# Kernel tuning notes

Measured on AMD Instinct MI355X. Metric: run time of the kernel, lower is better.

The kernel has to match this reference:

```python
import jax, jax.numpy as jnp
import numpy as np

N_EMB = 2048
EMB_DIM = 512
EPS_IN = 1e-5  # instance-norm epsilon (torch default used in instance_norm)


def setup_inputs() -> dict:
    key = jax.random.key(0)
    kx, ke = jax.random.split(key)
    x = jax.random.normal(kx, (32, 1024, EMB_DIM), dtype=jnp.float32)
    # codebook init: uniform(-1/M, 1/M), then row-normalized (as in __init__)
    init_bound = 1.0 / N_EMB
    emb = jax.random.uniform(ke, (N_EMB, EMB_DIM), dtype=jnp.float32,
                             minval=-init_bound, maxval=init_bound)
    emb = emb / (jnp.linalg.norm(emb, axis=1, keepdims=True) + 1e-4)
    return {"x": x, "embedding": emb}


def _instance_norm(x, axis, eps=EPS_IN):
    mu = jnp.mean(x, axis=axis, keepdims=True)
    # torch.std default is unbiased (ddof=1)
    std = jnp.std(x, axis=axis, keepdims=True, ddof=1)
    return (x - mu) / (std + eps)


def reference(x, embedding):
    N, T, D = x.shape
    M = embedding.shape[0]
    z = _instance_norm(x, axis=1)  # normalize over time dim

    # normalized codebook only used for distance computation
    emb_n = embedding / (jnp.linalg.norm(embedding, axis=1, keepdims=True) + 1e-4)

    z_flat = jax.lax.stop_gradient(z).reshape(-1, D)  # (N*T, D)
    # ||e||^2 + ||z||^2 - 2 z.e  (addmm with alpha=-2, beta=1)
    distances = (jnp.sum(emb_n ** 2, axis=1)[None, :]
                 + jnp.sum(z_flat ** 2, axis=1, keepdims=True)
                 - 2.0 * (z_flat @ emb_n.T))  # (N*T, M)
    indices = jnp.argmin(distances.astype(jnp.float32), axis=-1)  # (N*T,)

    # lookup uses the UN-normalized embedding buffer (as in original)
    quantized = embedding[indices].reshape(N, T, D)

    commitment_loss = jnp.mean((z - jax.lax.stop_gradient(quantized)) ** 2)

    quantized_ste = z + jax.lax.stop_gradient(quantized - z)
    quantized_out = (quantized_ste + quantized) / 2.0

    # avg_probs = mean of one-hot encodings == normalized histogram
    counts = jnp.zeros((M,), dtype=jnp.float32).at[indices].add(1.0)
    avg_probs = counts / z_flat.shape[0]
    perplexity = jnp.exp(-jnp.sum(avg_probs * jnp.log(avg_probs + 1e-10)))

    return quantized_out, commitment_loss, perplexity
```

## Files before the change

### kernel.cpp

```cpp
#include <hip/hip_runtime.h>

#define T_DIM 1024
#define D_DIM 512
#define M_CODES 2048
#define NT 32768
#define TOTAL 16777216

typedef _Float16 h2 __attribute__((ext_vector_type(2)));
typedef float f32x4 __attribute__((ext_vector_type(4)));
typedef unsigned int u32;

#define WS_MU    0
#define WS_S     65536
#define WS_CZ    131072
#define WS_CE    262144
#define WS_KEYS  270336
#define WS_EB    532480
#define WS_HIST  (532480 + 1048576)
#define WS_LPART (WS_HIST + 8192)

__device__ __forceinline__ void gload16(const void* g, void* l) {
    __builtin_amdgcn_global_load_lds(
        (const __attribute__((address_space(1))) u32*)g,
        (__attribute__((address_space(3))) u32*)l, 16, 0, 0);
}

__device__ __forceinline__ float block_reduce_sum_256(float v) {
    #pragma unroll
    for (int s = 32; s; s >>= 1) v += __shfl_xor(v, s, 64);
    __shared__ float ls[4];
    int w = threadIdx.x >> 6;
    if ((threadIdx.x & 63) == 0) ls[w] = v;
    __syncthreads();
    float r = (ls[0] + ls[1]) + (ls[2] + ls[3]);
    __syncthreads();
    return r;
}

__device__ __forceinline__ u32 pk_fp8x4(float a, float b, float c, float d) {
    u32 w = __builtin_amdgcn_cvt_pk_fp8_f32(a, b, 0, false);
    w = __builtin_amdgcn_cvt_pk_fp8_f32(c, d, w, true);
    return w;
}

__global__ void stats_kernel(const float* __restrict__ x,
                             float* __restrict__ mu_o, float* __restrict__ s_o) {
    int n = blockIdx.y;
    int lane = threadIdx.x & 63;
    int d = blockIdx.x * 64 + lane;
    int tg = threadIdx.x >> 6;
    const float* xp = x + (size_t)n * (T_DIM * D_DIM) + d;
    float sum = 0.f, sq = 0.f;
    int t0 = tg * 256;
    for (int it = 0; it < 256; ++it) {
        float v = xp[(size_t)(t0 + it) * D_DIM];
        sum += v; sq += v * v;
    }
    __shared__ float ssum[4][64], ssq[4][64];
    ssum[tg][lane] = sum;
    ssq[tg][lane] = sq;
    __syncthreads();
    if (threadIdx.x < 64) {
        int l = threadIdx.x;
        float s1 = (ssum[0][l] + ssum[1][l]) + (ssum[2][l] + ssum[3][l]);
        float q1 = (ssq[0][l] + ssq[1][l]) + (ssq[2][l] + ssq[3][l]);
        float mu = s1 * (1.0f / 1024.0f);
        float var = (q1 - 1024.0f * mu * mu) * (1.0f / 1023.0f);
        var = fmaxf(var, 0.0f);
        float sd = sqrtf(var) + 1e-5f;
        int nd = n * D_DIM + blockIdx.x * 64 + l;
        mu_o[nd] = mu; s_o[nd] = sd;
    }
}

__global__ void codebook_kernel(const float* __restrict__ emb,
                                unsigned char* __restrict__ eb, float* __restrict__ ce) {
    int j = blockIdx.x;
    int d = threadIdx.x * 2;
    float2 e = *(const float2*)&emb[(size_t)j * D_DIM + d];
    float sq = e.x * e.x + e.y * e.y;
    float norm2 = block_reduce_sum_256(sq);
    float den = sqrtf(norm2) + 1e-4f;
    float en0 = e.x / den, en1 = e.y / den;
    u32 w = __builtin_amdgcn_cvt_pk_fp8_f32(en0, en1, 0, false);
    *(unsigned short*)&eb[(size_t)j * D_DIM + d] = (unsigned short)(w & 0xFFFF);
    float cep = en0 * en0 + en1 * en1;
    float cesum = block_reduce_sum_256(cep);
    if (threadIdx.x == 0) ce[j] = cesum;
}

__global__ void cz_split_kernel(const float* __restrict__ x, const float* __restrict__ mu,
                                const float* __restrict__ s, float* __restrict__ cz,
                                unsigned char* __restrict__ zq) {
    int i = blockIdx.x * 4 + (threadIdx.x >> 6);
    int lane = threadIdx.x & 63;
    int n = i >> 10;
    const float* xp = x + (size_t)i * D_DIM;
    const float* mp = mu + n * D_DIM;
    const float* sp = s + n * D_DIM;
    float acc = 0.f;
    #pragma unroll
    for (int c = 0; c < 2; ++c) {
        int d = c * 256 + lane * 4;
        float4 xv = *(const float4*)&xp[d];
        float4 mv = *(const float4*)&mp[d];
        float4 sv = *(const float4*)&sp[d];
        float z0 = (xv.x - mv.x) / sv.x;
        float z1 = (xv.y - mv.y) / sv.y;
        float z2 = (xv.z - mv.z) / sv.z;
        float z3 = (xv.w - mv.w) / sv.w;
        *(u32*)&zq[(size_t)i * D_DIM + d] = pk_fp8x4(z0, z1, z2, z3);
        acc += z0 * z0 + z1 * z1 + z2 * z2 + z3 * z3;
    }
    #pragma unroll
    for (int sft = 32; sft; sft >>= 1) acc += __shfl_xor(acc, sft, 64);
    if (lane == 0) cz[i] = acc;
}

__global__ __launch_bounds__(512, 2) void gemm_argmin(
    const unsigned char* __restrict__ zq, const unsigned char* __restrict__ eb,
    const float* __restrict__ ce, const float* __restrict__ cz,
    unsigned long long* __restrict__ keys) {
    __shared__ long smem[2][4096];
    int tid = threadIdx.x;
    int bid = blockIdx.x;
    int swz = (bid & 7) * 128 + (bid >> 3);
    int n0 = (swz & 7) * 256;
    int m0 = (swz >> 3) * 256;

    f32x4 acc[4][8];
    #pragma unroll
    for (int a = 0; a < 4; ++a)
        #pragma unroll
        for (int b = 0; b < 8; ++b) acc[a][b] = (f32x4)0.0f;

    int w = tid >> 6, l = tid & 63;
    int wm = (w >> 1) * 64;
    int wn = (w & 1) * 128;
    int fr = l & 15, fg = l >> 4;

    #define STAGE(buf, kc) do {                                                   \
        _Pragma("unroll")                                                         \
        for (int q = 0; q < 2; ++q) {                                             \
            int r = 32 * w + 16 * q + (l >> 2);                                   \
            int c = (((l & 3) ^ ((r >> 1) & 3)) << 4);                            \
            char* dA = (char*)&smem[buf][0]    + (32 * w + 16 * q) * 64;          \
            char* dB = (char*)&smem[buf][2048] + (32 * w + 16 * q) * 64;          \
            gload16(zq + (size_t)(m0 + r) * D_DIM + (kc) + c, dA);                \
            gload16(eb + (size_t)(n0 + r) * D_DIM + (kc) + c, dB);                \
        }                                                                         \
    } while (0)

    STAGE(0, 0);
    __syncthreads();

    int cur = 0;
    for (int t = 0; t < 8; ++t) {
        if (t < 7) STAGE(cur ^ 1, (t + 1) * 64);
        long av[4][2], bv[8][2];
        #pragma unroll
        for (int i = 0; i < 4; ++i) {
            int r = wm + i * 16 + fr;
            int xr = (r >> 1) & 3;
            #pragma unroll
            for (int h = 0; h < 2; ++h) {
                int sl = ((h << 1) + (fg >> 1)) ^ xr;
                av[i][h] = smem[cur][r * 8 + sl * 2 + (fg & 1)];
            }
        }
        #pragma unroll
        for (int j = 0; j < 8; ++j) {
            int r = wn + j * 16 + fr;
            int xr = (r >> 1) & 3;
            #pragma unroll
            for (int h = 0; h < 2; ++h) {
                int sl = ((h << 1) + (fg >> 1)) ^ xr;
                bv[j][h] = smem[cur][2048 + r * 8 + sl * 2 + (fg & 1)];
            }
        }
        __builtin_amdgcn_s_setprio(1);
        #pragma unroll
        for (int mb = 0; mb < 4; ++mb)
            #pragma unroll
            for (int nb = 0; nb < 8; ++nb) {
                acc[mb][nb] = __builtin_amdgcn_mfma_f32_16x16x32_fp8_fp8(
                    av[mb][0], bv[nb][0], acc[mb][nb], 0, 0, 0);
                acc[mb][nb] = __builtin_amdgcn_mfma_f32_16x16x32_fp8_fp8(
                    av[mb][1], bv[nb][1], acc[mb][nb], 0, 0, 0);
            }
        __builtin_amdgcn_s_setprio(0);
        __syncthreads();
        cur ^= 1;
    }
    #undef STAGE

    #pragma unroll
    for (int mb = 0; mb < 4; ++mb) {
        #pragma unroll
        for (int r = 0; r < 4; ++r) {
            int q = m0 + wm + mb * 16 + fg * 4 + r;
            float czq = cz[q];
            unsigned long long best = ~0ULL;
            #pragma unroll
            for (int nb = 0; nb < 8; ++nb) {
                int j = n0 + wn + nb * 16 + fr;
                float dist = (ce[j] + czq) - 2.0f * acc[mb][nb][r];
                unsigned long long key =
                    ((unsigned long long)__float_as_uint(dist) << 32) | (unsigned)j;
                if (key < best) best = key;
            }
            #pragma unroll
            for (int sft = 1; sft < 16; sft <<= 1) {
                unsigned long long o = __shfl_xor(best, sft, 64);
                if (o < best) best = o;
            }
            if (fr == 0) atomicMin(keys + q, best);
        }
    }
}

__global__ void output_kernel(const float* __restrict__ x, const float* __restrict__ mu,
                              const float* __restrict__ s, const float* __restrict__ emb,
                              const unsigned long long* __restrict__ keys,
                              float* __restrict__ out, float* __restrict__ loss_part,
                              unsigned* __restrict__ hist) {
    int i = blockIdx.x * 4 + (threadIdx.x >> 6);
    int lane = threadIdx.x & 63;
    int n = i >> 10;
    unsigned idx = (unsigned)(keys[i] & 0xFFFFFFFFULL);
    float lsum = 0.f;
    #pragma unroll
    for (int c = 0; c < 2; ++c) {
        int d = c * 256 + lane * 4;
        float4 xv = *(const float4*)&x[(size_t)i * D_DIM + d];
        float4 mv = *(const float4*)&mu[n * D_DIM + d];
        float4 sv = *(const float4*)&s[n * D_DIM + d];
        float4 ev = *(const float4*)&emb[(size_t)idx * D_DIM + d];
        float z0 = (xv.x - mv.x) / sv.x;
        float z1 = (xv.y - mv.y) / sv.y;
        float z2 = (xv.z - mv.z) / sv.z;
        float z3 = (xv.w - mv.w) / sv.w;
        float o0 = ((z0 + (ev.x - z0)) + ev.x) * 0.5f;
        float o1 = ((z1 + (ev.y - z1)) + ev.y) * 0.5f;
        float o2 = ((z2 + (ev.z - z2)) + ev.z) * 0.5f;
        float o3 = ((z3 + (ev.w - z3)) + ev.w) * 0.5f;
        *(float4*)&out[(size_t)i * D_DIM + d] = make_float4(o0, o1, o2, o3);
        lsum += (z0 - ev.x) * (z0 - ev.x) + (z1 - ev.y) * (z1 - ev.y)
              + (z2 - ev.z) * (z2 - ev.z) + (z3 - ev.w) * (z3 - ev.w);
    }
    #pragma unroll
    for (int sft = 32; sft; sft >>= 1) lsum += __shfl_xor(lsum, sft, 64);
    __shared__ float ls[4];
    if (lane == 0) {
        ls[threadIdx.x >> 6] = lsum;
        atomicAdd(&hist[idx], 1u);
    }
    __syncthreads();
    if (threadIdx.x == 0)
        loss_part[blockIdx.x] = (ls[0] + ls[1]) + (ls[2] + ls[3]);
}

__global__ void final_kernel(const unsigned* __restrict__ hist,
                             const float* __restrict__ loss_part, float* __restrict__ out) {
    float h = 0.f;
    for (int b = threadIdx.x; b < M_CODES; b += 256) {
        float p = (float)hist[b] * (1.0f / 32768.0f);
        h += p * logf(p + 1e-10f);
    }
    h = block_reduce_sum_256(h);
    float lsum = 0.f;
    for (int b = threadIdx.x; b < NT / 4; b += 256) lsum += loss_part[b];
    lsum = block_reduce_sum_256(lsum);
    if (threadIdx.x == 0) {
        out[TOTAL] = lsum * (1.0f / 16777216.0f);
        out[TOTAL + 1] = expf(-h);
    }
}

extern "C" void kernel_launch(void* const* d_in, const int* in_sizes, int n_in,
                              void* d_out, int out_size, void* d_ws, size_t ws_size,
                              hipStream_t stream) {
    (void)in_sizes; (void)n_in; (void)out_size; (void)ws_size;
    const float* x = (const float*)d_in[0];
    const float* emb = (const float*)d_in[1];
    float* out = (float*)d_out;
    char* ws = (char*)d_ws;
    float* mu   = (float*)(ws + WS_MU);
    float* s    = (float*)(ws + WS_S);
    float* cz   = (float*)(ws + WS_CZ);
    float* ce   = (float*)(ws + WS_CE);
    unsigned long long* keys = (unsigned long long*)(ws + WS_KEYS);
    unsigned char* eb = (unsigned char*)(ws + WS_EB);
    unsigned* hist = (unsigned*)(ws + WS_HIST);
    float* loss_part = (float*)(ws + WS_LPART);
    unsigned char* zq = (unsigned char*)d_out;

    (void)hipMemsetAsync(ws + WS_KEYS, 0xFF, 262144, stream);
    (void)hipMemsetAsync(ws + WS_HIST, 0x00, 8192, stream);

    stats_kernel<<<dim3(8, 32), 256, 0, stream>>>(x, mu, s);
    codebook_kernel<<<M_CODES, 256, 0, stream>>>(emb, eb, ce);
    cz_split_kernel<<<NT / 4, 256, 0, stream>>>(x, mu, s, cz, zq);
    gemm_argmin<<<1024, 512, 0, stream>>>(zq, eb, ce, cz, keys);
    output_kernel<<<NT / 4, 256, 0, stream>>>(x, mu, s, emb, keys, out, loss_part, hist);
    final_kernel<<<1, 256, 0, stream>>>(hist, loss_part, out);
}
```

Before: 169.1 us.

## Pre-swizzle fp8 operands in global memory and use 4-stage LDS pipeline

The producer kernels now write the fp8 z and codebook rows in a pre-swizzled column order, so the GEMM can copy contiguous 16-byte chunks straight into LDS and read conflict-free fragments without per-load XOR math. The GEMM main loop moves from a double-buffered 64-wide K step to a 4-deep ring of 32-wide K steps with explicit vmcnt waits and raw barriers, keeping three loads in flight. This aims to hide global-to-LDS latency and cut address arithmetic, at the cost of more barriers per K and halved MFMA work per stage.

```diff
diff --git a/kernel.cpp b/kernel.cpp
--- a/kernel.cpp
+++ b/kernel.cpp
@@ -6,7 +6,6 @@
 #define NT 32768
 #define TOTAL 16777216
 
-typedef _Float16 h2 __attribute__((ext_vector_type(2)));
 typedef float f32x4 __attribute__((ext_vector_type(4)));
 typedef unsigned int u32;
 
@@ -41,6 +40,10 @@
     u32 w = __builtin_amdgcn_cvt_pk_fp8_f32(a, b, 0, false);
     w = __builtin_amdgcn_cvt_pk_fp8_f32(c, d, w, true);
     return w;
+}
+
+__device__ __forceinline__ int pk_dest(int d, int row) {
+    return (d & ~31) | ((((d >> 3) & 3) ^ ((row >> 2) & 3)) << 3) | (d & 7);
 }
 
 __global__ void stats_kernel(const float* __restrict__ x,
@@ -83,7 +86,8 @@
     float den = sqrtf(norm2) + 1e-4f;
     float en0 = e.x / den, en1 = e.y / den;
     u32 w = __builtin_amdgcn_cvt_pk_fp8_f32(en0, en1, 0, false);
-    *(unsigned short*)&eb[(size_t)j * D_DIM + d] = (unsigned short)(w & 0xFFFF);
+    *(unsigned short*)&eb[(size_t)j * D_DIM + pk_dest(d, j)] =
+        (unsigned short)(w & 0xFFFF);
     float cep = en0 * en0 + en1 * en1;
     float cesum = block_reduce_sum_256(cep);
     if (threadIdx.x == 0) ce[j] = cesum;
@@ -109,7 +113,7 @@
         float z1 = (xv.y - mv.y) / sv.y;
         float z2 = (xv.z - mv.z) / sv.z;
         float z3 = (xv.w - mv.w) / sv.w;
-        *(u32*)&zq[(size_t)i * D_DIM + d] = pk_fp8x4(z0, z1, z2, z3);
+        *(u32*)&zq[(size_t)i * D_DIM + pk_dest(d, i)] = pk_fp8x4(z0, z1, z2, z3);
         acc += z0 * z0 + z1 * z1 + z2 * z2 + z3 * z3;
     }
     #pragma unroll
@@ -121,7 +125,7 @@
     const unsigned char* __restrict__ zq, const unsigned char* __restrict__ eb,
     const float* __restrict__ ce, const float* __restrict__ cz,
     unsigned long long* __restrict__ keys) {
-    __shared__ long smem[2][4096];
+    __shared__ long smem[4][2048];
     int tid = threadIdx.x;
     int bid = blockIdx.x;
     int swz = (bid & 7) * 128 + (bid >> 3);
@@ -138,59 +142,50 @@
     int wm = (w >> 1) * 64;
     int wn = (w & 1) * 128;
     int fr = l & 15, fg = l >> 4;
-
-    #define STAGE(buf, kc) do {                                                   \
-        _Pragma("unroll")                                                         \
-        for (int q = 0; q < 2; ++q) {                                             \
-            int r = 32 * w + 16 * q + (l >> 2);                                   \
-            int c = (((l & 3) ^ ((r >> 1) & 3)) << 4);                            \
-            char* dA = (char*)&smem[buf][0]    + (32 * w + 16 * q) * 64;          \
-            char* dB = (char*)&smem[buf][2048] + (32 * w + 16 * q) * 64;          \
-            gload16(zq + (size_t)(m0 + r) * D_DIM + (kc) + c, dA);                \
-            gload16(eb + (size_t)(n0 + r) * D_DIM + (kc) + c, dB);                \
-        }                                                                         \
+    int xfg = fg ^ ((fr >> 2) & 3);
+
+    int rS = 32 * w + (l >> 1);
+    int hS = (l & 1) * 16;
+    size_t srcA = (size_t)(m0 + rS) * D_DIM + hS;
+    size_t srcB = (size_t)(n0 + rS) * D_DIM + hS;
+
+    #define STAGE(buf, t) do {                                                    \
+        gload16(zq + srcA + (t) * 32, &smem[buf][w * 128]);                       \
+        gload16(eb + srcB + (t) * 32, &smem[buf][1024 + w * 128]);                \
     } while (0)
 
     STAGE(0, 0);
-    __syncthreads();
-
-    int cur = 0;
-    for (int t = 0; t < 8; ++t) {
-        if (t < 7) STAGE(cur ^ 1, (t + 1) * 64);
-        long av[4][2], bv[8][2];
-        #pragma unroll
-        for (int i = 0; i < 4; ++i) {
-            int r = wm + i * 16 + fr;
-            int xr = (r >> 1) & 3;
-            #pragma unroll
-            for (int h = 0; h < 2; ++h) {
-                int sl = ((h << 1) + (fg >> 1)) ^ xr;
-                av[i][h] = smem[cur][r * 8 + sl * 2 + (fg & 1)];
-            }
-        }
-        #pragma unroll
-        for (int j = 0; j < 8; ++j) {
-            int r = wn + j * 16 + fr;
-            int xr = (r >> 1) & 3;
-            #pragma unroll
-            for (int h = 0; h < 2; ++h) {
-                int sl = ((h << 1) + (fg >> 1)) ^ xr;
-                bv[j][h] = smem[cur][2048 + r * 8 + sl * 2 + (fg & 1)];
-            }
-        }
+    STAGE(1, 1);
+    STAGE(2, 2);
+    asm volatile("s_waitcnt vmcnt(4)" ::: "memory");
+    __builtin_amdgcn_s_barrier();
+    __builtin_amdgcn_sched_barrier(0);
+
+    for (int t = 0; t < 16; ++t) {
+        int cur = t & 3;
+        if (t <= 12) STAGE((t + 3) & 3, t + 3);
+        long av[4], bv[8];
+        #pragma unroll
+        for (int i = 0; i < 4; ++i)
+            av[i] = smem[cur][(wm + i * 16 + fr) * 4 + xfg];
+        #pragma unroll
+        for (int j = 0; j < 8; ++j)
+            bv[j] = smem[cur][1024 + (wn + j * 16 + fr) * 4 + xfg];
         __builtin_amdgcn_s_setprio(1);
         #pragma unroll
         for (int mb = 0; mb < 4; ++mb)
             #pragma unroll
-            for (int nb = 0; nb < 8; ++nb) {
+            for (int nb = 0; nb < 8; ++nb)
                 acc[mb][nb] = __builtin_amdgcn_mfma_f32_16x16x32_fp8_fp8(
-                    av[mb][0], bv[nb][0], acc[mb][nb], 0, 0, 0);
-                acc[mb][nb] = __builtin_amdgcn_mfma_f32_16x16x32_fp8_fp8(
-                    av[mb][1], bv[nb][1], acc[mb][nb], 0, 0, 0);
-            }
+                    av[mb], bv[nb], acc[mb][nb], 0, 0, 0);
         __builtin_amdgcn_s_setprio(0);
-        __syncthreads();
-        cur ^= 1;
+        if (t < 15) {
+            if (t <= 12)      asm volatile("s_waitcnt vmcnt(4)" ::: "memory");
+            else if (t == 13) asm volatile("s_waitcnt vmcnt(2)" ::: "memory");
+            else              asm volatile("s_waitcnt vmcnt(0)" ::: "memory");
+            __builtin_amdgcn_s_barrier();
+            __builtin_amdgcn_sched_barrier(0);
+        }
     }
     #undef STAGE
 
```

After: 165.1 us. -2.4%, faster.
